# Kernel tuning notes

Hardware: AMD Instinct MI355X
Metric: run time of the kernel (lower is better)

Reference implementation:

```python
import jax, jax.numpy as jnp
import numpy as np

B, S, D = 8, 1024, 768
H, DK, DV = 12, 64, 64


def setup_inputs() -> dict:
    key = jax.random.key(0)
    ks = jax.random.split(key, 8)
    s_in = 1.0 / np.sqrt(D)
    s_cat = 1.0 / np.sqrt(H * DV)
    return {
        "x": jax.random.normal(ks[0], (B, S, D), jnp.float32),
        "Wq": jax.random.normal(ks[1], (H, D, DK), jnp.float32) * s_in,
        "bq": jnp.zeros((H, DK), jnp.float32),
        "Wk": jax.random.normal(ks[2], (H, D, DK), jnp.float32) * s_in,
        "bk": jnp.zeros((H, DK), jnp.float32),
        "Wv": jax.random.normal(ks[3], (H, D, DV), jnp.float32) * s_in,
        "bv": jnp.zeros((H, DV), jnp.float32),
        "W0": jax.random.normal(ks[4], (H * DV, D), jnp.float32) * s_cat,
        "b0": jnp.zeros((D,), jnp.float32),
    }


def reference(x, Wq, bq, Wk, bk, Wv, bv, W0, b0):
    # Per-head projections, batched across heads (same math as the ModuleList loop).
    q = jnp.einsum("bsd,hdk->bhsk", x, Wq) + bq[None, :, None, :]  # [B,H,S,DK]
    k = jnp.einsum("bsd,hdk->bhsk", x, Wk) + bk[None, :, None, :]
    v = jnp.einsum("bsd,hdv->bhsv", x, Wv) + bv[None, :, None, :]
    scale = 1.0 / jnp.sqrt(jnp.asarray(DK, x.dtype))
    scores = jnp.einsum("bhqk,bhsk->bhqs", q, k) * scale  # [B,H,S,S]
    causal = jnp.tril(jnp.ones((S, S), bool))
    scores = jnp.where(causal[None, None], scores, jnp.asarray(-1e9, x.dtype))
    attn = jax.nn.softmax(scores, axis=-1)
    out = jnp.einsum("bhqs,bhsv->bhqv", attn, v)  # [B,H,S,DV]
    # concat heads along last dim -> [B,S,H*DV]
    out = jnp.transpose(out, (0, 2, 1, 3)).reshape(B, S, H * DV)
    # output projection (dropout is identity in eval mode / p=0)
    return out @ W0 + b0
```

## Files before the change

### kernel.cpp

```cpp
#include <hip/hip_runtime.h>


typedef __attribute__((ext_vector_type(8))) short short8;
typedef __attribute__((ext_vector_type(4))) float f32x4;

#define Bsz 8
#define Ssz 1024
#define Dsz 768
#define Hsz 12
#define DKsz 64
#define KVB 128

__device__ __forceinline__ short f2bf(float f) {
    unsigned u = __float_as_uint(f);
    u = (u + 0x7fffu + ((u >> 16) & 1u)) >> 16;
    return (short)u;
}

__device__ __forceinline__ float fexp2(float x) {
    float r;
    asm("v_exp_f32 %0, %1" : "=v"(r) : "v"(x));
    return r;
}

__device__ __forceinline__ f32x4 mfma16(short8 a, short8 b, f32x4 c) {
    return __builtin_amdgcn_mfma_f32_16x16x32_bf16(a, b, c, 0, 0, 0);
}

__device__ __forceinline__ void gload16(const short* g, short* lds) {
    __builtin_amdgcn_global_load_lds(
        (const __attribute__((address_space(1))) void*)g,
        (__attribute__((address_space(3))) void*)lds, 16, 0, 0);
}

__global__ __launch_bounds__(256) void cast_x_kernel(const float* __restrict__ x,
                                                     short* __restrict__ xbf) {
    int i = (blockIdx.x * 256 + threadIdx.x) * 8;
    float4 a = *reinterpret_cast<const float4*>(&x[i]);
    float4 b = *reinterpret_cast<const float4*>(&x[i + 4]);
    short8 o;
    o[0] = f2bf(a.x); o[1] = f2bf(a.y); o[2] = f2bf(a.z); o[3] = f2bf(a.w);
    o[4] = f2bf(b.x); o[5] = f2bf(b.y); o[6] = f2bf(b.z); o[7] = f2bf(b.w);
    *reinterpret_cast<short8*>(&xbf[i]) = o;
}

__global__ __launch_bounds__(256) void pack_qkvw_kernel(const float* __restrict__ Wq,
                                                        const float* __restrict__ Wk,
                                                        const float* __restrict__ Wv,
                                                        short* __restrict__ Wt) {
    int idx = blockIdx.x * 256 + threadIdx.x;
    int n = idx / Dsz;
    int k = idx % Dsz;
    int which = n / 768;
    int hc = n - which * 768;
    int h = hc >> 6, c = hc & 63;
    const float* W = (which == 0) ? Wq : (which == 1) ? Wk : Wv;
    Wt[idx] = f2bf(W[(h * Dsz + k) * DKsz + c]);
}

__global__ __launch_bounds__(256) void pack_w0_kernel(const float* __restrict__ W0,
                                                      short* __restrict__ W0t) {
    int idx = blockIdx.x * 256 + threadIdx.x;
    int n = idx / Dsz;
    int k = idx % Dsz;
    W0t[idx] = f2bf(W0[k * Dsz + n]);
}

#define GEMM_MAIN(A_, Bt_, Kdim)                                                   \
    int tid = threadIdx.x, w = tid >> 6, l = tid & 63;                             \
    int wr = w >> 1, wc = w & 1;                                                   \
    int lr = l & 15, lg = l >> 4;                                                  \
    __shared__ short Als[128 * 32];                                                \
    __shared__ short Bls[128 * 32];                                                \
    f32x4 acc[4][4] = {};                                                          \
    for (int k0 = 0; k0 < (Kdim); k0 += 32) {                                      \
        __syncthreads();                                                           \
        _Pragma("unroll")                                                          \
        for (int j = 0; j < 2; ++j) {                                              \
            int i = j * 256 + w * 64 + l;                                          \
            gload16((A_) + (i >> 2) * (Kdim) + k0 + (i & 3) * 8,                   \
                    &Als[(j * 256 + w * 64) * 8]);                                 \
            gload16((Bt_) + (i >> 2) * (Kdim) + k0 + (i & 3) * 8,                  \
                    &Bls[(j * 256 + w * 64) * 8]);                                 \
        }                                                                          \
        __syncthreads();                                                           \
        short8 af[4], bf[4];                                                       \
        _Pragma("unroll")                                                          \
        for (int m = 0; m < 4; ++m)                                                \
            af[m] = *reinterpret_cast<const short8*>(                              \
                &Als[(wr * 64 + m * 16 + lr) * 32 + lg * 8]);                      \
        _Pragma("unroll")                                                          \
        for (int n = 0; n < 4; ++n)                                                \
            bf[n] = *reinterpret_cast<const short8*>(                              \
                &Bls[(wc * 64 + n * 16 + lr) * 32 + lg * 8]);                      \
        _Pragma("unroll")                                                          \
        for (int m = 0; m < 4; ++m)                                                \
            _Pragma("unroll")                                                      \
            for (int n = 0; n < 4; ++n)                                            \
                acc[m][n] = mfma16(af[m], bf[n], acc[m][n]);                       \
    }

__global__ __launch_bounds__(256) void gemm_qkv_kernel(
    const short* __restrict__ A, const short* __restrict__ Bt,
    const float* __restrict__ bq, const float* __restrict__ bk,
    const float* __restrict__ bv,
    short* __restrict__ Qb, short* __restrict__ Kb, short* __restrict__ Vb) {
    int tn = blockIdx.x % 18, tm = blockIdx.x / 18;
    const short* Ab = A + (size_t)tm * 128 * Dsz;
    const short* Bb = Bt + (size_t)tn * 128 * Dsz;
    GEMM_MAIN(Ab, Bb, Dsz)
    int which = tn / 6;
    const float* bias = (which == 0) ? bq : (which == 1) ? bk : bv;
    short* dst = (which == 0) ? Qb : (which == 1) ? Kb : Vb;
    int row0 = tm * 128 + wr * 64;
    int col0 = tn * 128 + wc * 64 - which * 768;
#pragma unroll
    for (int m = 0; m < 4; ++m)
#pragma unroll
        for (int n = 0; n < 4; ++n)
#pragma unroll
            for (int j = 0; j < 4; ++j) {
                int row = row0 + m * 16 + lg * 4 + j;
                int col = col0 + n * 16 + lr;
                int b = row >> 10, s = row & 1023;
                int h = col >> 6, c = col & 63;
                float v = acc[m][n][j] + bias[h * 64 + c];
                if (which == 0) v *= 0.180336884f;
                size_t addr = (which == 2)
                    ? ((((size_t)b * Hsz + h) * DKsz + c) * Ssz + s)
                    : ((((size_t)b * Hsz + h) * Ssz + s) * DKsz + c);
                dst[addr] = f2bf(v);
            }
}

__global__ __launch_bounds__(256) void attn_kernel(const short* __restrict__ Q,
                                                   const short* __restrict__ K,
                                                   const short* __restrict__ Vt,
                                                   short* __restrict__ O) {
    int raw = blockIdx.x;
    int xcd = raw & 7, slot = raw >> 3;
    int bh  = (slot >> 4) * 8 + xcd;
    int qb  = 15 - (slot & 15);
    const short* Qh = Q + (size_t)bh * Ssz * DKsz;
    const short* Kh = K + (size_t)bh * Ssz * DKsz;
    const short* Vh = Vt + (size_t)bh * DKsz * Ssz;
    int tid = threadIdx.x, w = tid >> 6, l = tid & 63;
    int lr = l & 15, lg = l >> 4;
    __shared__ short Kls[KVB * 64];
    __shared__ short Vls[64 * KVB];
    __shared__ short Pls[4][16 * KVB];

    int qrow = qb * 64 + w * 16 + lr;
    short8 aq0 = *reinterpret_cast<const short8*>(&Qh[qrow * 64 + lg * 8]);
    short8 aq1 = *reinterpret_cast<const short8*>(&Qh[qrow * 64 + 32 + lg * 8]);

    short8 ones;
#pragma unroll
    for (int e = 0; e < 8; ++e) ones[e] = (short)0x3F80;

    f32x4 acc[4] = {};
    f32x4 accL = {};

    int nt = qb / 2 + 1;
    for (int t = 0; t < nt; ++t) {
        __syncthreads();
        const short* Ksrc = Kh + t * KVB * 64;
#pragma unroll
        for (int it = 0; it < 4; ++it) {
            int i = it * 256 + tid;
            int r = i >> 3, ps = i & 7;
            gload16(Ksrc + r * 64 + ((ps ^ (r & 7)) << 3),
                    &Kls[(it * 256 + w * 64) * 8]);
        }
#pragma unroll
        for (int it = 0; it < 4; ++it) {
            int i = it * 256 + tid;
            int r = i >> 4, ps = i & 15;
            gload16(Vh + r * Ssz + t * KVB + ((ps ^ (r & 15)) << 3),
                    &Vls[(it * 256 + w * 64) * 8]);
        }
        __syncthreads();

        f32x4 s[8] = {};
        __builtin_amdgcn_s_setprio(1);
#pragma unroll
        for (int n = 0; n < 8; ++n) {
            int kr = n * 16 + lr;
            short8 kf0 = *reinterpret_cast<const short8*>(
                &Kls[kr * 64 + ((lg ^ (kr & 7)) << 3)]);
            short8 kf1 = *reinterpret_cast<const short8*>(
                &Kls[kr * 64 + (((lg + 4) ^ (kr & 7)) << 3)]);
            s[n] = mfma16(aq0, kf0, s[n]);
            s[n] = mfma16(aq1, kf1, s[n]);
        }
        __builtin_amdgcn_s_setprio(0);

        if (t == nt - 1) {
#pragma unroll
            for (int n = 0; n < 8; ++n)
#pragma unroll
                for (int j = 0; j < 4; ++j) {
                    int kv = t * KVB + n * 16 + lr;
                    int q = qb * 64 + w * 16 + lg * 4 + j;
                    if (kv > q) s[n][j] = -1e30f;
                }
        }

#pragma unroll
        for (int n = 0; n < 8; ++n)
#pragma unroll
            for (int j = 0; j < 4; ++j) {
                float p = fexp2(s[n][j]);
                int row = lg * 4 + j;
                int col = n * 16 + lr;
                Pls[w][row * KVB + (col ^ (row << 3))] = f2bf(p);
            }

        __builtin_amdgcn_s_setprio(1);
#pragma unroll
        for (int kk = 0; kk < 4; ++kk) {
            int sl = (((kk * 4 + lg) ^ lr) << 3);
            short8 pa = *reinterpret_cast<const short8*>(&Pls[w][lr * KVB + sl]);
            accL = mfma16(pa, ones, accL);
#pragma unroll
            for (int n = 0; n < 4; ++n) {
                short8 vf = *reinterpret_cast<const short8*>(
                    &Vls[(n * 16 + lr) * KVB + sl]);
                acc[n] = mfma16(pa, vf, acc[n]);
            }
        }
        __builtin_amdgcn_s_setprio(0);
    }

    int b = bh / Hsz, h = bh % Hsz;
#pragma unroll
    for (int n = 0; n < 4; ++n)
#pragma unroll
        for (int j = 0; j < 4; ++j) {
            int q = qb * 64 + w * 16 + lg * 4 + j;
            int dv = n * 16 + lr;
            float o = acc[n][j] / accL[j];
            O[((size_t)(b * Ssz + q)) * Dsz + h * DKsz + dv] = f2bf(o);
        }
}

__global__ __launch_bounds__(256) void gemm_out_kernel(const short* __restrict__ A,
                                                       const short* __restrict__ Bt,
                                                       const float* __restrict__ b0,
                                                       float* __restrict__ out) {
    int tn = blockIdx.x % 6, tm = blockIdx.x / 6;
    const short* Ab = A + (size_t)tm * 128 * Dsz;
    const short* Bb = Bt + (size_t)tn * 128 * Dsz;
    GEMM_MAIN(Ab, Bb, Dsz)
    int row0 = tm * 128 + wr * 64;
    int col0 = tn * 128 + wc * 64;
#pragma unroll
    for (int m = 0; m < 4; ++m)
#pragma unroll
        for (int n = 0; n < 4; ++n)
#pragma unroll
            for (int j = 0; j < 4; ++j) {
                int row = row0 + m * 16 + lg * 4 + j;
                int col = col0 + n * 16 + lr;
                out[(size_t)row * Dsz + col] = acc[m][n][j] + b0[col];
            }
}

extern "C" void kernel_launch(void* const* d_in, const int* in_sizes, int n_in,
                              void* d_out, int out_size, void* d_ws, size_t ws_size,
                              hipStream_t stream) {
    const float* x  = (const float*)d_in[0];
    const float* Wq = (const float*)d_in[1];
    const float* bq = (const float*)d_in[2];
    const float* Wk = (const float*)d_in[3];
    const float* bk = (const float*)d_in[4];
    const float* Wv = (const float*)d_in[5];
    const float* bv = (const float*)d_in[6];
    const float* W0 = (const float*)d_in[7];
    const float* b0 = (const float*)d_in[8];
    float* out = (float*)d_out;

    const size_t N_X   = (size_t)Bsz * Ssz * Dsz;
    const size_t N_QKV = (size_t)3 * Dsz * Dsz;
    const size_t N_W0  = (size_t)Dsz * Dsz;
    const size_t N_HD  = (size_t)Bsz * Hsz * Ssz * DKsz;

    short* xbf   = (short*)d_ws;
    short* wqkvt = xbf + N_X;
    short* w0t   = wqkvt + N_QKV;
    short* Qb    = w0t + N_W0;
    short* Kb    = Qb + N_HD;
    short* Vb    = Kb + N_HD;
    short* attno = Vb + N_HD;

    cast_x_kernel<<<(int)(N_X / 2048), 256, 0, stream>>>(x, xbf);
    pack_qkvw_kernel<<<(int)(N_QKV / 256), 256, 0, stream>>>(Wq, Wk, Wv, wqkvt);
    pack_w0_kernel<<<(int)(N_W0 / 256), 256, 0, stream>>>(W0, w0t);
    gemm_qkv_kernel<<<64 * 18, 256, 0, stream>>>(xbf, wqkvt, bq, bk, bv, Qb, Kb, Vb);
    attn_kernel<<<Bsz * Hsz * 16, 256, 0, stream>>>(Qb, Kb, Vb, attno);
    gemm_out_kernel<<<64 * 6, 256, 0, stream>>>(attno, w0t, b0, out);
}
```

Measured before the change: 239.9 us.

## Double-buffer GEMM LDS, swizzle tiles, remap blocks to XCDs, vectorize V stores

The shared GEMM macro now uses two LDS buffers, so the next K-slice is fetched while the current one feeds the MFMAs, cutting one barrier per iteration. LDS tiles get an XOR swizzle to avoid bank conflicts. Both projection GEMMs remap block IDs so each XCD works on a contiguous run of tiles for better L2 reuse. The V output writes 4 consecutive sequence values as one packed store. The cost is twice the LDS per block, which may lower occupancy.

Measured after the change: 231.1 us. -3.6%, faster.

```diff
diff --git a/kernel.cpp b/kernel.cpp
--- a/kernel.cpp
+++ b/kernel.cpp
@@ -2,6 +2,7 @@
 
 
 typedef __attribute__((ext_vector_type(8))) short short8;
+typedef __attribute__((ext_vector_type(4))) short short4_t;
 typedef __attribute__((ext_vector_type(4))) float f32x4;
 
 #define Bsz 8
@@ -70,67 +71,98 @@
     int tid = threadIdx.x, w = tid >> 6, l = tid & 63;                             \
     int wr = w >> 1, wc = w & 1;                                                   \
     int lr = l & 15, lg = l >> 4;                                                  \
-    __shared__ short Als[128 * 32];                                                \
-    __shared__ short Bls[128 * 32];                                                \
+    __shared__ short Als[2][128 * 32];                                             \
+    __shared__ short Bls[2][128 * 32];                                             \
     f32x4 acc[4][4] = {};                                                          \
-    for (int k0 = 0; k0 < (Kdim); k0 += 32) {                                      \
-        __syncthreads();                                                           \
+    auto STAGE = [&](int cb, int k0) {                                             \
         _Pragma("unroll")                                                          \
         for (int j = 0; j < 2; ++j) {                                              \
             int i = j * 256 + w * 64 + l;                                          \
-            gload16((A_) + (i >> 2) * (Kdim) + k0 + (i & 3) * 8,                   \
-                    &Als[(j * 256 + w * 64) * 8]);                                 \
-            gload16((Bt_) + (i >> 2) * (Kdim) + k0 + (i & 3) * 8,                  \
-                    &Bls[(j * 256 + w * 64) * 8]);                                 \
+            int r = i >> 2, sl = i & 3;                                            \
+            gload16((A_) + r * (Kdim) + k0 + ((sl ^ (r & 3)) << 3),                \
+                    &Als[cb][(j * 256 + w * 64) * 8]);                             \
+            gload16((Bt_) + r * (Kdim) + k0 + ((sl ^ (r & 3)) << 3),               \
+                    &Bls[cb][(j * 256 + w * 64) * 8]);                             \
         }                                                                          \
-        __syncthreads();                                                           \
+    };                                                                             \
+    auto COMPUTE = [&](int cb) {                                                   \
         short8 af[4], bf[4];                                                       \
         _Pragma("unroll")                                                          \
-        for (int m = 0; m < 4; ++m)                                                \
+        for (int m = 0; m < 4; ++m) {                                              \
+            int row = wr * 64 + m * 16 + lr;                                       \
             af[m] = *reinterpret_cast<const short8*>(                              \
-                &Als[(wr * 64 + m * 16 + lr) * 32 + lg * 8]);                      \
+                &Als[cb][row * 32 + ((lg ^ (row & 3)) << 3)]);                     \
+        }                                                                          \
         _Pragma("unroll")                                                          \
-        for (int n = 0; n < 4; ++n)                                                \
+        for (int n = 0; n < 4; ++n) {                                              \
+            int row = wc * 64 + n * 16 + lr;                                       \
             bf[n] = *reinterpret_cast<const short8*>(                              \
-                &Bls[(wc * 64 + n * 16 + lr) * 32 + lg * 8]);                      \
+                &Bls[cb][row * 32 + ((lg ^ (row & 3)) << 3)]);                     \
+        }                                                                          \
         _Pragma("unroll")                                                          \
         for (int m = 0; m < 4; ++m)                                                \
             _Pragma("unroll")                                                      \
             for (int n = 0; n < 4; ++n)                                            \
                 acc[m][n] = mfma16(af[m], bf[n], acc[m][n]);                       \
-    }
+    };                                                                             \
+    int cur = 0;                                                                   \
+    STAGE(0, 0);                                                                   \
+    __syncthreads();                                                               \
+    for (int k0 = 32; k0 < (Kdim); k0 += 32) {                                     \
+        STAGE(cur ^ 1, k0);                                                        \
+        COMPUTE(cur);                                                              \
+        __syncthreads();                                                           \
+        cur ^= 1;                                                                  \
+    }                                                                              \
+    COMPUTE(cur);
 
 __global__ __launch_bounds__(256) void gemm_qkv_kernel(
     const short* __restrict__ A, const short* __restrict__ Bt,
     const float* __restrict__ bq, const float* __restrict__ bk,
     const float* __restrict__ bv,
     short* __restrict__ Qb, short* __restrict__ Kb, short* __restrict__ Vb) {
-    int tn = blockIdx.x % 18, tm = blockIdx.x / 18;
+    int tile = (blockIdx.x & 7) * 144 + (blockIdx.x >> 3);
+    int tm = tile / 18, tn = tile % 18;
     const short* Ab = A + (size_t)tm * 128 * Dsz;
     const short* Bb = Bt + (size_t)tn * 128 * Dsz;
     GEMM_MAIN(Ab, Bb, Dsz)
     int which = tn / 6;
     const float* bias = (which == 0) ? bq : (which == 1) ? bk : bv;
-    short* dst = (which == 0) ? Qb : (which == 1) ? Kb : Vb;
     int row0 = tm * 128 + wr * 64;
     int col0 = tn * 128 + wc * 64 - which * 768;
-#pragma unroll
-    for (int m = 0; m < 4; ++m)
-#pragma unroll
-        for (int n = 0; n < 4; ++n)
-#pragma unroll
-            for (int j = 0; j < 4; ++j) {
-                int row = row0 + m * 16 + lg * 4 + j;
+    if (which == 2) {
+#pragma unroll
+        for (int m = 0; m < 4; ++m)
+#pragma unroll
+            for (int n = 0; n < 4; ++n) {
+                int s0 = row0 + m * 16 + lg * 4;
                 int col = col0 + n * 16 + lr;
-                int b = row >> 10, s = row & 1023;
+                int b = s0 >> 10, s = s0 & 1023;
                 int h = col >> 6, c = col & 63;
-                float v = acc[m][n][j] + bias[h * 64 + c];
-                if (which == 0) v *= 0.180336884f;
-                size_t addr = (which == 2)
-                    ? ((((size_t)b * Hsz + h) * DKsz + c) * Ssz + s)
-                    : ((((size_t)b * Hsz + h) * Ssz + s) * DKsz + c);
-                dst[addr] = f2bf(v);
+                float bi = bias[h * 64 + c];
+                short4_t pk;
+#pragma unroll
+                for (int j = 0; j < 4; ++j) pk[j] = f2bf(acc[m][n][j] + bi);
+                *reinterpret_cast<short4_t*>(
+                    &Vb[(((size_t)b * Hsz + h) * DKsz + c) * Ssz + s]) = pk;
             }
+    } else {
+        short* dst = (which == 0) ? Qb : Kb;
+#pragma unroll
+        for (int m = 0; m < 4; ++m)
+#pragma unroll
+            for (int n = 0; n < 4; ++n)
+#pragma unroll
+                for (int j = 0; j < 4; ++j) {
+                    int row = row0 + m * 16 + lg * 4 + j;
+                    int col = col0 + n * 16 + lr;
+                    int b = row >> 10, s = row & 1023;
+                    int h = col >> 6, c = col & 63;
+                    float v = acc[m][n][j] + bias[h * 64 + c];
+                    if (which == 0) v *= 0.180336884f;
+                    dst[(((size_t)b * Hsz + h) * Ssz + s) * DKsz + c] = f2bf(v);
+                }
+    }
 }
 
 __global__ __launch_bounds__(256) void attn_kernel(const short* __restrict__ Q,
@@ -248,7 +280,8 @@
                                                        const short* __restrict__ Bt,
                                                        const float* __restrict__ b0,
                                                        float* __restrict__ out) {
-    int tn = blockIdx.x % 6, tm = blockIdx.x / 6;
+    int tile = (blockIdx.x & 7) * 48 + (blockIdx.x >> 3);
+    int tm = tile / 6, tn = tile % 6;
     const short* Ab = A + (size_t)tm * 128 * Dsz;
     const short* Bb = Bt + (size_t)tn * 128 * Dsz;
     GEMM_MAIN(Ab, Bb, Dsz)
```
